# Kernel optimization log

Measured on AMD Instinct MI355X. Metric: run time of the kernel, lower is better.

Reference implementation:

```python
import jax, jax.numpy as jnp
import numpy as np

B, S, D = 4, 2048, 1024

def setup_inputs() -> dict:
    key = jax.random.key(0)
    k1, k2, k3, k4 = jax.random.split(key, 4)
    output = jax.random.normal(k1, (B, S, D), dtype=jnp.float32)
    # nn.Linear(dim, dim, bias=False): y = x @ W.T ; store W as [D, D]
    scale = 1.0 / np.sqrt(D)
    w_q = jax.random.uniform(k2, (D, D), dtype=jnp.float32, minval=-scale, maxval=scale)
    w_k = jax.random.uniform(k3, (D, D), dtype=jnp.float32, minval=-scale, maxval=scale)
    w_v = jax.random.uniform(k4, (D, D), dtype=jnp.float32, minval=-scale, maxval=scale)
    return {"output": output, "w_q": w_q, "w_k": w_k, "w_v": w_v}

def reference(output, w_q, w_k, w_v):
    # projections: x @ W.T (torch Linear convention)
    q = jnp.einsum('bsd,ed->bse', output, w_q)
    k = jnp.einsum('bsd,ed->bse', output, w_k)
    v = jnp.einsum('bsd,ed->bse', output, w_v)
    scores = jnp.einsum('bqd,bkd->bqk', q, k)      # unscaled, no mask
    attn = jax.nn.softmax(scores, axis=-1)
    return jnp.einsum('bqk,bkd->bqd', attn, v)
```

## Files before the change

kernel.cpp:

```cpp
#include <hip/hip_runtime.h>
#include <hip/hip_bf16.h>
#include <stdint.h>


typedef __attribute__((ext_vector_type(8))) _Float16 f16x8;
typedef __attribute__((ext_vector_type(4))) float f32x4;
typedef __attribute__((ext_vector_type(4))) unsigned short u16x4;

__device__ inline unsigned short f2h(float f) {
    union { _Float16 h; unsigned short u; } x;
    x.h = (_Float16)f;
    return x.u;
}
__device__ inline float h2f(unsigned short u) {
    union { unsigned short u; _Float16 h; } x;
    x.u = u;
    return (float)x.h;
}

__device__ inline void async16(const unsigned short* g, unsigned short* l) {
    __builtin_amdgcn_global_load_lds(
        (__attribute__((address_space(1))) void*)g,
        (__attribute__((address_space(3))) void*)l, 16, 0, 0);
}

template <int MODE, int BN>
__global__ __launch_bounds__(512)
void gemm512(const unsigned short* __restrict__ A,
             const unsigned short* __restrict__ B,
             void* __restrict__ C, void* __restrict__ C2,
             int K, int ldA, int ldB, int ldC,
             long sAz, long sBz, long sCz)
{
    constexpr int NT = BN / 32;
    constexpr int BI = BN / 64;
    __shared__ __align__(16) unsigned short smem[256 * 64 + BN * 64];
    unsigned short* As = smem;
    unsigned short* Bs = smem + 256 * 64;

    const int tid  = threadIdx.x;
    const int lane = tid & 63;
    const int wave = tid >> 6;
    const int wr   = wave >> 1, wc = wave & 1;
    const int quad = lane >> 4, lrow = lane & 15;
    const int bm   = blockIdx.x, bn = blockIdx.y, z = blockIdx.z;

    const unsigned short* Az = A + (long)z * sAz;
    const unsigned short* Bz = B + (long)z * sBz;

    const unsigned short* gA[4];
    const unsigned short* gB[BI];
#pragma unroll
    for (int i = 0; i < 4; ++i) {
        const int l = tid + 512 * i;
        const int r = l >> 3;
        const int c = (l & 7) ^ (r & 7);
        gA[i] = Az + (long)(bm * 256 + r) * ldA + c * 8;
    }
#pragma unroll
    for (int i = 0; i < BI; ++i) {
        const int l = tid + 512 * i;
        const int r = l >> 3;
        const int c = (l & 7) ^ (r & 7);
        gB[i] = Bz + (long)(bn * BN + r) * ldB + c * 8;
    }

    f32x4 acc[4][NT];
#pragma unroll
    for (int i = 0; i < 4; ++i)
#pragma unroll
        for (int j = 0; j < NT; ++j)
            acc[i][j] = f32x4{0.f, 0.f, 0.f, 0.f};

    const int fr = lrow & 7;

    for (int k0 = 0; k0 < K; k0 += 64) {
#pragma unroll
        for (int i = 0; i < 4; ++i) async16(gA[i], &As[(tid + 512 * i) * 8]);
#pragma unroll
        for (int i = 0; i < BI; ++i) async16(gB[i], &Bs[(tid + 512 * i) * 8]);
#pragma unroll
        for (int i = 0; i < 4; ++i) gA[i] += 64;
#pragma unroll
        for (int i = 0; i < BI; ++i) gB[i] += 64;
        __syncthreads();

#pragma unroll
        for (int ks = 0; ks < 2; ++ks) {
            const int pc = (((ks << 2) + quad) ^ fr) * 8;
            f16x8 af[4], bf[NT];
#pragma unroll
            for (int mt = 0; mt < 4; ++mt)
                af[mt] = *(const f16x8*)&As[(wr * 64 + mt * 16 + lrow) * 64 + pc];
#pragma unroll
            for (int nt = 0; nt < NT; ++nt)
                bf[nt] = *(const f16x8*)&Bs[(wc * (BN / 2) + nt * 16 + lrow) * 64 + pc];
#pragma unroll
            for (int mt = 0; mt < 4; ++mt)
#pragma unroll
                for (int nt = 0; nt < NT; ++nt)
                    acc[mt][nt] = __builtin_amdgcn_mfma_f32_16x16x32_f16(
                        af[mt], bf[nt], acc[mt][nt], 0, 0, 0);
        }
        __syncthreads();
    }

    const int col_base = bn * BN + wc * (BN / 2);

    if (MODE != 0 || z < 2) {
        const int row_base = bm * 256 + wr * 64;
        const long zC = (long)z * sCz;
#pragma unroll
        for (int mt = 0; mt < 4; ++mt)
#pragma unroll
            for (int nt = 0; nt < NT; ++nt)
#pragma unroll
                for (int r = 0; r < 4; ++r) {
                    const int row = row_base + mt * 16 + quad * 4 + r;
                    const int col = col_base + nt * 16 + lrow;
                    if (MODE == 2)
                        ((float*)C)[zC + (long)row * ldC + col] = acc[mt][nt][r];
                    else
                        ((unsigned short*)C)[zC + (long)row * ldC + col] =
                            f2h(acc[mt][nt][r]);
                }
    } else {
        unsigned short* T = smem;
#pragma unroll
        for (int p = 0; p < 4; ++p) {
            __syncthreads();
            if (wr == p) {
#pragma unroll
                for (int mt = 0; mt < 4; ++mt)
#pragma unroll
                    for (int nt = 0; nt < NT; ++nt) {
                        const int row_l = mt * 16 + quad * 4;
                        const int col_l = wc * 64 + nt * 16 + lrow;
                        u16x4 pk = {f2h(acc[mt][nt][0]), f2h(acc[mt][nt][1]),
                                    f2h(acc[mt][nt][2]), f2h(acc[mt][nt][3])};
                        *(u16x4*)&T[col_l * 72 + row_l] = pk;
                    }
            }
            __syncthreads();
            const int c  = tid >> 2;
            const int j0 = (tid & 3) * 16;
            const int tok0 = bm * 256 + p * 64;
            const int bb = tok0 >> 11;
            const int s0 = (tok0 & 2047) + j0;
            unsigned short* dst = (unsigned short*)C2 + (long)bb * 2097152 +
                                  (long)(bn * 128 + c) * 2048 + s0;
            const unsigned short* srcT = &T[c * 72 + j0];
            *(f16x8*)dst = *(const f16x8*)srcT;
            *(f16x8*)(dst + 8) = *(const f16x8*)(srcT + 8);
        }
    }
}

__global__ __launch_bounds__(256)
void cvt_all(const float* __restrict__ x, const float* __restrict__ w0,
             const float* __restrict__ w1, const float* __restrict__ w2,
             unsigned short* __restrict__ xh, unsigned short* __restrict__ wh)
{
    const int bid = blockIdx.x;
    const float* s;
    unsigned short* d;
    long i;
    if (bid < 4096) {
        s = x; d = xh;
        i = ((long)bid * 256 + threadIdx.x) * 8;
    } else {
        const int wid = bid - 4096;
        const int w = wid >> 9;
        s = (w == 0) ? w0 : (w == 1) ? w1 : w2;
        d = wh + (long)w * 1048576;
        i = ((long)(wid & 511) * 256 + threadIdx.x) * 8;
    }
    f32x4 a = *(const f32x4*)(s + i);
    f32x4 b = *(const f32x4*)(s + i + 4);
    union { unsigned short u[8]; f16x8 v; } t;
#pragma unroll
    for (int j = 0; j < 4; ++j) { t.u[j] = f2h(a[j]); t.u[4 + j] = f2h(b[j]); }
    *(f16x8*)(d + i) = t.v;
}

__global__ __launch_bounds__(256)
void softmax16(unsigned short* __restrict__ sc)
{
    const long row = blockIdx.x;
    unsigned short* srow = sc + row * 2048;
    const int tid = threadIdx.x;

    union { u16x4 p[2]; unsigned short u[8]; } in;
    in.p[0] = *(const u16x4*)(srow + tid * 8);
    in.p[1] = *(const u16x4*)(srow + tid * 8 + 4);
    float v[8];
#pragma unroll
    for (int i = 0; i < 8; ++i) v[i] = h2f(in.u[i]);

    float m = v[0];
#pragma unroll
    for (int i = 1; i < 8; ++i) m = fmaxf(m, v[i]);
#pragma unroll
    for (int off = 32; off; off >>= 1) m = fmaxf(m, __shfl_xor(m, off));

    __shared__ float redm[4], reds[4];
    if ((tid & 63) == 0) redm[tid >> 6] = m;
    __syncthreads();
    m = fmaxf(fmaxf(redm[0], redm[1]), fmaxf(redm[2], redm[3]));

    float s = 0.f;
#pragma unroll
    for (int i = 0; i < 8; ++i) { v[i] = __expf(v[i] - m); s += v[i]; }
#pragma unroll
    for (int off = 32; off; off >>= 1) s += __shfl_xor(s, off);
    if ((tid & 63) == 0) reds[tid >> 6] = s;
    __syncthreads();
    s = reds[0] + reds[1] + reds[2] + reds[3];

    const float inv = 1.f / s;
    union { unsigned short u[8]; f16x8 w; } t;
#pragma unroll
    for (int i = 0; i < 8; ++i) t.u[i] = f2h(v[i] * inv);
    *(f16x8*)(srow + tid * 8) = t.w;
}

extern "C" void kernel_launch(void* const* d_in, const int* in_sizes, int n_in,
                              void* d_out, int out_size, void* d_ws, size_t ws_size,
                              hipStream_t stream)
{
    const float* x  = (const float*)d_in[0];
    const float* wq = (const float*)d_in[1];
    const float* wk = (const float*)d_in[2];
    const float* wv = (const float*)d_in[3];
    float* out = (float*)d_out;

    char* base = (char*)d_ws;
    const bool batched = (ws_size >= 88080384UL);

    unsigned short* xh = (unsigned short*)base;
    unsigned short* wh = (unsigned short*)(base + 16777216);
    unsigned short* sc = (unsigned short*)base;
    unsigned short* q  = (unsigned short*)(base + (batched ? 33554432 : 23068672));
    unsigned short* k  = q + 8388608;
    unsigned short* vt = k + 8388608;

    cvt_all<<<5632, 256, 0, stream>>>(x, wq, wk, wv, xh, wh);

    gemm512<0, 128><<<dim3(32, 8, 3), 512, 0, stream>>>(
        xh, wh, q, vt, 1024, 1024, 1024, 1024, 0L, 1048576L, 8388608L);

    if (batched) {
        gemm512<1, 128><<<dim3(8, 16, 4), 512, 0, stream>>>(
            q, k, sc, nullptr, 1024, 1024, 1024, 2048,
            2097152L, 2097152L, 4194304L);
        softmax16<<<8192, 256, 0, stream>>>(sc);
        gemm512<2, 64><<<dim3(8, 16, 4), 512, 0, stream>>>(
            sc, vt, out, nullptr, 2048, 2048, 2048, 1024,
            4194304L, 2097152L, 2097152L);
    } else {
        for (int b = 0; b < 4; ++b) {
            gemm512<1, 128><<<dim3(8, 16, 1), 512, 0, stream>>>(
                q + (long)b * 2097152, k + (long)b * 2097152, sc, nullptr,
                1024, 1024, 1024, 2048, 0L, 0L, 0L);
            softmax16<<<2048, 256, 0, stream>>>(sc);
            gemm512<2, 64><<<dim3(8, 16, 1), 512, 0, stream>>>(
                sc, vt + (long)b * 2097152, out + (long)b * 2097152, nullptr,
                2048, 2048, 2048, 1024, 0L, 0L, 0L);
        }
    }
}
```

Baseline: 231.8 us.

## Double-buffer GEMM LDS tiles with staggered async loads and split MFMA phases

```diff
diff --git a/kernel.cpp b/kernel.cpp
--- a/kernel.cpp
+++ b/kernel.cpp
@@ -1,5 +1,4 @@
 #include <hip/hip_runtime.h>
-#include <hip/hip_bf16.h>
 #include <stdint.h>
 
 
@@ -32,11 +31,11 @@
              int K, int ldA, int ldB, int ldC,
              long sAz, long sBz, long sCz)
 {
+    static_assert(BN == 128, "pipeline is derived for BN=128");
     constexpr int NT = BN / 32;
     constexpr int BI = BN / 64;
-    __shared__ __align__(16) unsigned short smem[256 * 64 + BN * 64];
-    unsigned short* As = smem;
-    unsigned short* Bs = smem + 256 * 64;
+    constexpr int TILE = 256 * 64 + BN * 64;
+    __shared__ __align__(16) unsigned short smem[2 * TILE];
 
     const int tid  = threadIdx.x;
     const int lane = tid & 63;
@@ -73,36 +72,95 @@
             acc[i][j] = f32x4{0.f, 0.f, 0.f, 0.f};
 
     const int fr = lrow & 7;
-
-    for (int k0 = 0; k0 < K; k0 += 64) {
-#pragma unroll
-        for (int i = 0; i < 4; ++i) async16(gA[i], &As[(tid + 512 * i) * 8]);
-#pragma unroll
-        for (int i = 0; i < BI; ++i) async16(gB[i], &Bs[(tid + 512 * i) * 8]);
-#pragma unroll
-        for (int i = 0; i < 4; ++i) gA[i] += 64;
-#pragma unroll
-        for (int i = 0; i < BI; ++i) gB[i] += 64;
-        __syncthreads();
-
+    const int ntiles = K >> 6;
+
+#pragma unroll
+    for (int i = 0; i < 4; ++i)
+        async16(gA[i], &smem[(tid + 512 * i) * 8]);
+#pragma unroll
+    for (int i = 0; i < BI; ++i)
+        async16(gB[i], &smem[256 * 64 + (tid + 512 * i) * 8]);
+#pragma unroll
+    for (int i = 0; i < 4; ++i) {
+        async16(gA[i] + 64, &smem[TILE + (tid + 512 * i) * 8]);
+        gA[i] += 128;
+    }
+#pragma unroll
+    for (int i = 0; i < BI; ++i) gB[i] += 64;
+
+    asm volatile("s_waitcnt vmcnt(4)" ::: "memory");
+    __builtin_amdgcn_s_barrier();
+
+    for (int t = 0; t < ntiles; ++t) {
+        const unsigned short* cA = smem + (t & 1) * TILE;
+        const unsigned short* cB = cA + 256 * 64;
+        unsigned short* nxt  = smem + ((t + 1) & 1) * TILE;
+        unsigned short* cur  = smem + (t & 1) * TILE;
+
+        f16x8 af[4][2], b0f[2][2];
 #pragma unroll
         for (int ks = 0; ks < 2; ++ks) {
             const int pc = (((ks << 2) + quad) ^ fr) * 8;
-            f16x8 af[4], bf[NT];
 #pragma unroll
             for (int mt = 0; mt < 4; ++mt)
-                af[mt] = *(const f16x8*)&As[(wr * 64 + mt * 16 + lrow) * 64 + pc];
-#pragma unroll
-            for (int nt = 0; nt < NT; ++nt)
-                bf[nt] = *(const f16x8*)&Bs[(wc * (BN / 2) + nt * 16 + lrow) * 64 + pc];
-#pragma unroll
-            for (int mt = 0; mt < 4; ++mt)
-#pragma unroll
-                for (int nt = 0; nt < NT; ++nt)
-                    acc[mt][nt] = __builtin_amdgcn_mfma_f32_16x16x32_f16(
-                        af[mt], bf[nt], acc[mt][nt], 0, 0, 0);
-        }
-        __syncthreads();
+                af[mt][ks] = *(const f16x8*)&cA[(wr * 64 + mt * 16 + lrow) * 64 + pc];
+#pragma unroll
+            for (int n = 0; n < 2; ++n)
+                b0f[n][ks] = *(const f16x8*)&cB[(wc * (BN / 2) + n * 16 + lrow) * 64 + pc];
+        }
+        if (t + 1 < ntiles) {
+#pragma unroll
+            for (int i = 0; i < BI; ++i) {
+                async16(gB[i], &nxt[256 * 64 + (tid + 512 * i) * 8]);
+                gB[i] += 64;
+            }
+        }
+        __builtin_amdgcn_s_barrier();
+        asm volatile("s_waitcnt lgkmcnt(0)");
+        __builtin_amdgcn_s_setprio(1);
+#pragma unroll
+        for (int mt = 0; mt < 4; ++mt)
+#pragma unroll
+            for (int n = 0; n < 2; ++n)
+#pragma unroll
+                for (int ks = 0; ks < 2; ++ks)
+                    acc[mt][n] = __builtin_amdgcn_mfma_f32_16x16x32_f16(
+                        af[mt][ks], b0f[n][ks], acc[mt][n], 0, 0, 0);
+        __builtin_amdgcn_s_setprio(0);
+        __builtin_amdgcn_s_barrier();
+
+        f16x8 b1f[2][2];
+#pragma unroll
+        for (int ks = 0; ks < 2; ++ks) {
+            const int pc = (((ks << 2) + quad) ^ fr) * 8;
+#pragma unroll
+            for (int n = 0; n < 2; ++n)
+                b1f[n][ks] = *(const f16x8*)&cB[(wc * (BN / 2) + (2 + n) * 16 + lrow) * 64 + pc];
+        }
+        if (t + 2 < ntiles) {
+#pragma unroll
+            for (int i = 0; i < 4; ++i) {
+                async16(gA[i], &cur[(tid + 512 * i) * 8]);
+                gA[i] += 64;
+            }
+        }
+        __builtin_amdgcn_s_barrier();
+        asm volatile("s_waitcnt lgkmcnt(0)");
+        __builtin_amdgcn_s_setprio(1);
+#pragma unroll
+        for (int mt = 0; mt < 4; ++mt)
+#pragma unroll
+            for (int n = 0; n < 2; ++n)
+#pragma unroll
+                for (int ks = 0; ks < 2; ++ks)
+                    acc[mt][2 + n] = __builtin_amdgcn_mfma_f32_16x16x32_f16(
+                        af[mt][ks], b1f[n][ks], acc[mt][2 + n], 0, 0, 0);
+        __builtin_amdgcn_s_setprio(0);
+        if (t + 2 < ntiles)
+            asm volatile("s_waitcnt vmcnt(4)" ::: "memory");
+        else if (t + 1 < ntiles)
+            asm volatile("s_waitcnt vmcnt(0)" ::: "memory");
+        __builtin_amdgcn_s_barrier();
     }
 
     const int col_base = bn * BN + wc * (BN / 2);
@@ -254,7 +312,7 @@
             q, k, sc, nullptr, 1024, 1024, 1024, 2048,
             2097152L, 2097152L, 4194304L);
         softmax16<<<8192, 256, 0, stream>>>(sc);
-        gemm512<2, 64><<<dim3(8, 16, 4), 512, 0, stream>>>(
+        gemm512<2, 128><<<dim3(8, 8, 4), 512, 0, stream>>>(
             sc, vt, out, nullptr, 2048, 2048, 2048, 1024,
             4194304L, 2097152L, 2097152L);
     } else {
@@ -263,7 +321,7 @@
                 q + (long)b * 2097152, k + (long)b * 2097152, sc, nullptr,
                 1024, 1024, 1024, 2048, 0L, 0L, 0L);
             softmax16<<<2048, 256, 0, stream>>>(sc);
-            gemm512<2, 64><<<dim3(8, 16, 1), 512, 0, stream>>>(
+            gemm512<2, 128><<<dim3(8, 8, 1), 512, 0, stream>>>(
                 sc, vt + (long)b * 2097152, out + (long)b * 2097152, nullptr,
                 2048, 2048, 2048, 1024, 0L, 0L, 0L);
         }
```

New measurement: 250.3 us. +8.0%, slower.
